# Optimization experiments

Hardware: AMD Instinct MI355X
Metric: run time of the kernel (lower is better)

The kernel has to match this reference:

```python
import jax, jax.numpy as jnp
import numpy as np

N = 30          # n_particles
H = 32          # h_dim
D = 3           # input_dim
B = 1024        # batch of point clouds


def _make_edge_index():
    # fully connected, no self loops; rows = [source j, target i] (PyG convention)
    pairs = np.array([[m, n] for m in range(N) for n in range(N) if m != n], dtype=np.int64)
    return jnp.asarray(pairs.T)  # [2, 870]


def setup_inputs() -> dict:
    key = jax.random.key(0)
    ks = jax.random.split(key, 13)
    p = lambda k, shp: jax.random.normal(k, shp, dtype=jnp.float32) * 0.05
    return {
        "x": jax.random.normal(ks[0], (B, N, D), dtype=jnp.float32),
        "W1": p(ks[1], (2 * D, H)), "b1": p(ks[2], (H,)),
        "W2": p(ks[3], (H, H)),     "b2": p(ks[4], (H,)),
        "W3": p(ks[5], (H, H)),     "b3": p(ks[6], (H,)),
        "W4": p(ks[7], (2 * H, H)), "b4": p(ks[8], (H,)),
        "W5": p(ks[9], (H, H)),     "b5": p(ks[10], (H,)),
        "W6": p(ks[11], (H, D)),    "b6": p(ks[12], (D,)),
        "edge_index": _make_edge_index(),
    }


def _mlp(m, Wa, ba, Wb, bb, Wc, bc):
    h = jax.nn.relu(m @ Wa + ba)
    h = jax.nn.relu(h @ Wb + bb)
    return h @ Wc + bc


def _edge_conv(x, src, dst, Wa, ba, Wb, bb, Wc, bc):
    # x: [B, N, F]. PyG EdgeConv: msg = nn(cat[x_i, x_j - x_i]), mean over incoming edges at i.
    xi = x[:, dst]                               # [B, E, F]
    xj = x[:, src]                               # [B, E, F]
    msg = _mlp(jnp.concatenate([xi, xj - xi], axis=-1), Wa, ba, Wb, bb, Wc, bc)  # [B, E, Fout]
    n_nodes = x.shape[1]
    agg = jnp.zeros((x.shape[0], n_nodes, msg.shape[-1]), msg.dtype).at[:, dst].add(msg)
    cnt = jnp.zeros((n_nodes,), msg.dtype).at[dst].add(1.0)
    return agg / jnp.maximum(cnt, 1.0)[:, None]


def reference(x, W1, b1, W2, b2, W3, b3, W4, b4, W5, b5, W6, b6, edge_index):
    src, dst = edge_index[0], edge_index[1]
    h = _edge_conv(x, src, dst, W1, b1, W2, b2, W3, b3)   # [B, N, H]
    out = _edge_conv(h, src, dst, W4, b4, W5, b5, W6, b6)  # [B, N, D]
    return out
```

## Files before the change

### kernel.cpp

```cpp
#include <hip/hip_runtime.h>
#include <hip/hip_bf16.h>

namespace {

typedef __attribute__((ext_vector_type(8))) short short8;
typedef __attribute__((ext_vector_type(16))) float float16v;

constexpr int N = 30;
constexpr int H = 32;
constexpr int D = 3;
constexpr int PW = H + 4;
constexpr float INV_CNT = 1.0f / 29.0f;

__device__ __forceinline__ short bfb(float x) {
    __hip_bfloat16 h = __float2bfloat16(x);
    return __builtin_bit_cast(short, h);
}

__device__ __forceinline__ float16v mfma32(short8 a, short8 b, float16v c) {
    return __builtin_amdgcn_mfma_f32_32x32x16_bf16(a, b, c, 0, 0, 0);
}

__global__ __launch_bounds__(256, 4) void gnn2_v2(
    const float* __restrict__ x,
    const float* __restrict__ W1, const float* __restrict__ b1,
    const float* __restrict__ W2, const float* __restrict__ b2,
    const float* __restrict__ W3, const float* __restrict__ b3,
    const float* __restrict__ W4, const float* __restrict__ b4,
    const float* __restrict__ W5, const float* __restrict__ b5,
    const float* __restrict__ W6, const float* __restrict__ b6,
    float* __restrict__ out)
{
    __shared__ float uS[32 * PW];
    __shared__ float vS[32 * PW];
    __shared__ float aggS[32 * PW];
    __shared__ float t2S[4][32 * PW];

    const int b    = blockIdx.x;
    const int t    = threadIdx.x;
    const int lane = t & 63;
    const int w    = t >> 6;
    const int col  = lane & 31;
    const int h    = lane >> 5;
    const int j    = col;

    short8 W2lo, W2hi, W3lo, W3hi, W5lo, W5hi, W6lo, W6hi;
#pragma unroll
    for (int e = 0; e < 8; ++e) {
        const int klo = 8 * h + e, khi = 16 + 8 * h + e;
        W2lo[e] = bfb(W2[klo * H + col]);  W2hi[e] = bfb(W2[khi * H + col]);
        W3lo[e] = bfb(W3[klo * H + col]);  W3hi[e] = bfb(W3[khi * H + col]);
        W5lo[e] = bfb(W5[klo * H + col]);  W5hi[e] = bfb(W5[khi * H + col]);
        W6lo[e] = bfb(col < D ? W6[klo * D + col] : 0.0f);
        W6hi[e] = bfb(col < D ? W6[khi * D + col] : 0.0f);
    }
    const float bb2 = b2[col], bb5 = b5[col], b3c = b3[col];
    const float b6c = (col < D) ? b6[col] : 0.0f;

    const float* xb = x + b * (N * D);
    if (t < N * 8) {
        const int i = t >> 3, gg = t & 7;
        const float x0 = xb[i*D+0], x1 = xb[i*D+1], x2 = xb[i*D+2];
#pragma unroll
        for (int ff = 0; ff < 4; ++ff) {
            const int f = gg + 8 * ff;
            const float wa0 = W1[0*H+f], wa1 = W1[1*H+f], wa2 = W1[2*H+f];
            const float wb0 = W1[3*H+f], wb1 = W1[4*H+f], wb2 = W1[5*H+f];
            vS[i*PW+f] = x0*wb0 + x1*wb1 + x2*wb2;
            uS[i*PW+f] = x0*(wa0-wb0) + x1*(wa1-wb1) + x2*(wa2-wb2) + b1[f];
        }
    }
    __syncthreads();

    float* const rt = t2S[w];

    {
        float vlo[8], vhi[8];
#pragma unroll
        for (int e = 0; e < 8; ++e) {
            vlo[e] = vS[j*PW + 8*h + e];
            vhi[e] = vS[j*PW + 16 + 8*h + e];
        }
#pragma unroll 1
        for (int i = w; i < N; i += 4) {
            const bool alive = (j < N) && (j != i);
            const float* ur = &uS[i*PW];
            short8 alo, ahi;
#pragma unroll
            for (int e = 0; e < 8; ++e) {
                const float t0 = fmaxf(ur[8*h + e]      + vlo[e], 0.0f);
                const float t1 = fmaxf(ur[16 + 8*h + e] + vhi[e], 0.0f);
                alo[e] = alive ? bfb(t0) : (short)0;
                ahi[e] = alive ? bfb(t1) : (short)0;
            }
            float16v acc;
#pragma unroll
            for (int r = 0; r < 16; ++r) acc[r] = bb2;
            acc = mfma32(alo, W2lo, acc);
            acc = mfma32(ahi, W2hi, acc);
#pragma unroll
            for (int r = 0; r < 16; ++r)
                rt[((r&3) + 8*(r>>2) + 4*h) * PW + col] = fmaxf(acc[r], 0.0f);
            short8 clo, chi;
#pragma unroll
            for (int e = 0; e < 8; ++e) {
                const float t0 = rt[j*PW + 8*h + e];
                const float t1 = rt[j*PW + 16 + 8*h + e];
                clo[e] = alive ? bfb(t0) : (short)0;
                chi[e] = alive ? bfb(t1) : (short)0;
            }
            float16v a2;
#pragma unroll
            for (int r = 0; r < 16; ++r) a2[r] = 0.0f;
            a2 = mfma32(clo, W3lo, a2);
            a2 = mfma32(chi, W3hi, a2);
            float s = 0.0f;
#pragma unroll
            for (int r = 0; r < 16; ++r) s += a2[r];
            s += __shfl_xor(s, 32, 64);
            if (h == 0) aggS[i*PW + col] = s * INV_CNT + b3c;
        }
    }
    __syncthreads();

    if (w < 2) {
        const bool aliveC = (j < N);
        short8 alo, ahi;
#pragma unroll
        for (int e = 0; e < 8; ++e) {
            const float t0 = aggS[j*PW + 8*h + e];
            const float t1 = aggS[j*PW + 16 + 8*h + e];
            alo[e] = aliveC ? bfb(t0) : (short)0;
            ahi[e] = aliveC ? bfb(t1) : (short)0;
        }
        short8 Flo, Fhi;
        float binit;
        if (w == 0) {
#pragma unroll
            for (int e = 0; e < 8; ++e) {
                const int klo = 8*h + e, khi = 16 + 8*h + e;
                Flo[e] = bfb(W4[klo*H + col] - W4[(H + klo)*H + col]);
                Fhi[e] = bfb(W4[khi*H + col] - W4[(H + khi)*H + col]);
            }
            binit = b4[col];
        } else {
#pragma unroll
            for (int e = 0; e < 8; ++e) {
                const int klo = 8*h + e, khi = 16 + 8*h + e;
                Flo[e] = bfb(W4[(H + klo)*H + col]);
                Fhi[e] = bfb(W4[(H + khi)*H + col]);
            }
            binit = 0.0f;
        }
        float16v acc;
#pragma unroll
        for (int r = 0; r < 16; ++r) acc[r] = binit;
        acc = mfma32(alo, Flo, acc);
        acc = mfma32(ahi, Fhi, acc);
        float* const dst = (w == 0) ? uS : vS;
#pragma unroll
        for (int r = 0; r < 16; ++r)
            dst[((r&3) + 8*(r>>2) + 4*h) * PW + col] = acc[r];
    }
    __syncthreads();

    {
        float vlo[8], vhi[8];
#pragma unroll
        for (int e = 0; e < 8; ++e) {
            vlo[e] = vS[j*PW + 8*h + e];
            vhi[e] = vS[j*PW + 16 + 8*h + e];
        }
#pragma unroll 1
        for (int i = w; i < N; i += 4) {
            const bool alive = (j < N) && (j != i);
            const float* ur = &uS[i*PW];
            short8 alo, ahi;
#pragma unroll
            for (int e = 0; e < 8; ++e) {
                const float t0 = fmaxf(ur[8*h + e]      + vlo[e], 0.0f);
                const float t1 = fmaxf(ur[16 + 8*h + e] + vhi[e], 0.0f);
                alo[e] = alive ? bfb(t0) : (short)0;
                ahi[e] = alive ? bfb(t1) : (short)0;
            }
            float16v acc;
#pragma unroll
            for (int r = 0; r < 16; ++r) acc[r] = bb5;
            acc = mfma32(alo, W5lo, acc);
            acc = mfma32(ahi, W5hi, acc);
#pragma unroll
            for (int r = 0; r < 16; ++r)
                rt[((r&3) + 8*(r>>2) + 4*h) * PW + col] = fmaxf(acc[r], 0.0f);
            short8 clo, chi;
#pragma unroll
            for (int e = 0; e < 8; ++e) {
                const float t0 = rt[j*PW + 8*h + e];
                const float t1 = rt[j*PW + 16 + 8*h + e];
                clo[e] = alive ? bfb(t0) : (short)0;
                chi[e] = alive ? bfb(t1) : (short)0;
            }
            float16v a2;
#pragma unroll
            for (int r = 0; r < 16; ++r) a2[r] = 0.0f;
            a2 = mfma32(clo, W6lo, a2);
            a2 = mfma32(chi, W6hi, a2);
            float s = 0.0f;
#pragma unroll
            for (int r = 0; r < 16; ++r) s += a2[r];
            s += __shfl_xor(s, 32, 64);
            if (lane < D) out[b*(N*D) + i*D + lane] = s * INV_CNT + b6c;
        }
    }
}

}

extern "C" void kernel_launch(void* const* d_in, const int* in_sizes, int n_in,
                              void* d_out, int out_size, void* d_ws, size_t ws_size,
                              hipStream_t stream) {
    const float* x  = (const float*)d_in[0];
    const float* W1 = (const float*)d_in[1];
    const float* b1 = (const float*)d_in[2];
    const float* W2 = (const float*)d_in[3];
    const float* b2 = (const float*)d_in[4];
    const float* W3 = (const float*)d_in[5];
    const float* b3 = (const float*)d_in[6];
    const float* W4 = (const float*)d_in[7];
    const float* b4 = (const float*)d_in[8];
    const float* W5 = (const float*)d_in[9];
    const float* b5 = (const float*)d_in[10];
    const float* W6 = (const float*)d_in[11];
    const float* b6 = (const float*)d_in[12];

    const int batch = in_sizes[0] / (N * D);
    float* out = (float*)d_out;

    gnn2_v2<<<dim3(batch), dim3(256), 0, stream>>>(
        x, W1, b1, W2, b2, W3, b3, W4, b4, W5, b5, W6, b6, out);
}
```

Measured before the change: 111.4 us.

## Swap MFMA operand order and pass intermediate activations through lane shuffles, not LDS

```diff
diff --git a/kernel.cpp b/kernel.cpp
--- a/kernel.cpp
+++ b/kernel.cpp
@@ -3,8 +3,10 @@
 
 namespace {
 
-typedef __attribute__((ext_vector_type(8))) short short8;
+typedef __attribute__((ext_vector_type(8)))  short short8;
 typedef __attribute__((ext_vector_type(16))) float float16v;
+typedef __attribute__((ext_vector_type(4)))  float f4;
+typedef __attribute__((ext_vector_type(4)))  int   int4v;
 
 constexpr int N = 30;
 constexpr int H = 32;
@@ -16,12 +18,16 @@
     __hip_bfloat16 h = __float2bfloat16(x);
     return __builtin_bit_cast(short, h);
 }
-
+__device__ __forceinline__ int pkbf(float a, float b) {
+    const unsigned lo = (unsigned short)bfb(a);
+    const unsigned hi = (unsigned short)bfb(b);
+    return (int)(lo | (hi << 16));
+}
 __device__ __forceinline__ float16v mfma32(short8 a, short8 b, float16v c) {
     return __builtin_amdgcn_mfma_f32_32x32x16_bf16(a, b, c, 0, 0, 0);
 }
 
-__global__ __launch_bounds__(256, 4) void gnn2_v2(
+__global__ __launch_bounds__(256, 4) void gnn2_v3(
     const float* __restrict__ x,
     const float* __restrict__ W1, const float* __restrict__ b1,
     const float* __restrict__ W2, const float* __restrict__ b2,
@@ -34,7 +40,6 @@
     __shared__ float uS[32 * PW];
     __shared__ float vS[32 * PW];
     __shared__ float aggS[32 * PW];
-    __shared__ float t2S[4][32 * PW];
 
     const int b    = blockIdx.x;
     const int t    = threadIdx.x;
@@ -44,18 +49,17 @@
     const int h    = lane >> 5;
     const int j    = col;
 
-    short8 W2lo, W2hi, W3lo, W3hi, W5lo, W5hi, W6lo, W6hi;
+    short8 W2lo, W2hi, W3lo, W3hi;
 #pragma unroll
     for (int e = 0; e < 8; ++e) {
         const int klo = 8 * h + e, khi = 16 + 8 * h + e;
         W2lo[e] = bfb(W2[klo * H + col]);  W2hi[e] = bfb(W2[khi * H + col]);
         W3lo[e] = bfb(W3[klo * H + col]);  W3hi[e] = bfb(W3[khi * H + col]);
-        W5lo[e] = bfb(W5[klo * H + col]);  W5hi[e] = bfb(W5[khi * H + col]);
-        W6lo[e] = bfb(col < D ? W6[klo * D + col] : 0.0f);
-        W6hi[e] = bfb(col < D ? W6[khi * D + col] : 0.0f);
-    }
-    const float bb2 = b2[col], bb5 = b5[col], b3c = b3[col];
-    const float b6c = (col < D) ? b6[col] : 0.0f;
+    }
+    float b2v[16];
+#pragma unroll
+    for (int r = 0; r < 16; ++r) b2v[r] = b2[(r & 3) + 8 * (r >> 2) + 4 * h];
+    const float b3c = b3[col];
 
     const float* xb = x + b * (N * D);
     if (t < N * 8) {
@@ -70,53 +74,70 @@
             uS[i*PW+f] = x0*(wa0-wb0) + x1*(wa1-wb1) + x2*(wa2-wb2) + b1[f];
         }
     }
+    if (t < 2 * PW) {
+        uS[30*PW + t] = 0.0f;  vS[30*PW + t] = 0.0f;  aggS[30*PW + t] = 0.0f;
+    }
     __syncthreads();
 
-    float* const rt = t2S[w];
-
     {
-        float vlo[8], vhi[8];
-#pragma unroll
-        for (int e = 0; e < 8; ++e) {
-            vlo[e] = vS[j*PW + 8*h + e];
-            vhi[e] = vS[j*PW + 16 + 8*h + e];
-        }
+        const f4 v0 = *(const f4*)&vS[j*PW + 8*h];
+        const f4 v1 = *(const f4*)&vS[j*PW + 8*h + 4];
+        const f4 v2 = *(const f4*)&vS[j*PW + 16 + 8*h];
+        const f4 v3 = *(const f4*)&vS[j*PW + 16 + 8*h + 4];
 #pragma unroll 1
         for (int i = w; i < N; i += 4) {
             const bool alive = (j < N) && (j != i);
             const float* ur = &uS[i*PW];
-            short8 alo, ahi;
-#pragma unroll
-            for (int e = 0; e < 8; ++e) {
-                const float t0 = fmaxf(ur[8*h + e]      + vlo[e], 0.0f);
-                const float t1 = fmaxf(ur[16 + 8*h + e] + vhi[e], 0.0f);
-                alo[e] = alive ? bfb(t0) : (short)0;
-                ahi[e] = alive ? bfb(t1) : (short)0;
-            }
+            const f4 u0 = *(const f4*)(ur + 8*h);
+            const f4 u1 = *(const f4*)(ur + 8*h + 4);
+            const f4 u2 = *(const f4*)(ur + 16 + 8*h);
+            const f4 u3 = *(const f4*)(ur + 16 + 8*h + 4);
+            const short8 alo = __builtin_bit_cast(short8, (int4v){
+                pkbf(fmaxf(u0[0]+v0[0],0.f), fmaxf(u0[1]+v0[1],0.f)),
+                pkbf(fmaxf(u0[2]+v0[2],0.f), fmaxf(u0[3]+v0[3],0.f)),
+                pkbf(fmaxf(u1[0]+v1[0],0.f), fmaxf(u1[1]+v1[1],0.f)),
+                pkbf(fmaxf(u1[2]+v1[2],0.f), fmaxf(u1[3]+v1[3],0.f))});
+            const short8 ahi = __builtin_bit_cast(short8, (int4v){
+                pkbf(fmaxf(u2[0]+v2[0],0.f), fmaxf(u2[1]+v2[1],0.f)),
+                pkbf(fmaxf(u2[2]+v2[2],0.f), fmaxf(u2[3]+v2[3],0.f)),
+                pkbf(fmaxf(u3[0]+v3[0],0.f), fmaxf(u3[1]+v3[1],0.f)),
+                pkbf(fmaxf(u3[2]+v3[2],0.f), fmaxf(u3[3]+v3[3],0.f))});
             float16v acc;
 #pragma unroll
-            for (int r = 0; r < 16; ++r) acc[r] = bb2;
-            acc = mfma32(alo, W2lo, acc);
-            acc = mfma32(ahi, W2hi, acc);
-#pragma unroll
-            for (int r = 0; r < 16; ++r)
-                rt[((r&3) + 8*(r>>2) + 4*h) * PW + col] = fmaxf(acc[r], 0.0f);
-            short8 clo, chi;
-#pragma unroll
-            for (int e = 0; e < 8; ++e) {
-                const float t0 = rt[j*PW + 8*h + e];
-                const float t1 = rt[j*PW + 16 + 8*h + e];
-                clo[e] = alive ? bfb(t0) : (short)0;
-                chi[e] = alive ? bfb(t1) : (short)0;
-            }
-            float16v a2;
-#pragma unroll
-            for (int r = 0; r < 16; ++r) a2[r] = 0.0f;
-            a2 = mfma32(clo, W3lo, a2);
-            a2 = mfma32(chi, W3hi, a2);
+            for (int r = 0; r < 16; ++r) acc[r] = b2v[r];
+            acc = mfma32(W2lo, alo, acc);
+            acc = mfma32(W2hi, ahi, acc);
+            const int P0 = pkbf(fmaxf(acc[0], 0.f), fmaxf(acc[1], 0.f));
+            const int P1 = pkbf(fmaxf(acc[2], 0.f), fmaxf(acc[3], 0.f));
+            const int P2 = pkbf(fmaxf(acc[4], 0.f), fmaxf(acc[5], 0.f));
+            const int P3 = pkbf(fmaxf(acc[6], 0.f), fmaxf(acc[7], 0.f));
+            const int P4 = pkbf(fmaxf(acc[8], 0.f), fmaxf(acc[9], 0.f));
+            const int P5 = pkbf(fmaxf(acc[10],0.f), fmaxf(acc[11],0.f));
+            const int P6 = pkbf(fmaxf(acc[12],0.f), fmaxf(acc[13],0.f));
+            const int P7 = pkbf(fmaxf(acc[14],0.f), fmaxf(acc[15],0.f));
+            const int sp0 = __shfl_xor(P0, 32, 64);
+            const int sp1 = __shfl_xor(P1, 32, 64);
+            const int sp2 = __shfl_xor(P2, 32, 64);
+            const int sp3 = __shfl_xor(P3, 32, 64);
+            const int sp4 = __shfl_xor(P4, 32, 64);
+            const int sp5 = __shfl_xor(P5, 32, 64);
+            const int sp6 = __shfl_xor(P6, 32, 64);
+            const int sp7 = __shfl_xor(P7, 32, 64);
+            int w0 = h ? sp2 : P0;  int w1 = h ? sp3 : P1;
+            int w2 = h ? P2 : sp0;  int w3 = h ? P3 : sp1;
+            int w4 = h ? sp6 : P4;  int w5 = h ? sp7 : P5;
+            int w6 = h ? P6 : sp4;  int w7 = h ? P7 : sp5;
+            if (!alive) { w0=0; w1=0; w2=0; w3=0; w4=0; w5=0; w6=0; w7=0; }
+            const short8 a2lo = __builtin_bit_cast(short8, (int4v){w0, w1, w2, w3});
+            const short8 a2hi = __builtin_bit_cast(short8, (int4v){w4, w5, w6, w7});
+            float16v m2;
+#pragma unroll
+            for (int r = 0; r < 16; ++r) m2[r] = 0.0f;
+            m2 = mfma32(a2lo, W3lo, m2);
+            m2 = mfma32(a2hi, W3hi, m2);
             float s = 0.0f;
 #pragma unroll
-            for (int r = 0; r < 16; ++r) s += a2[r];
+            for (int r = 0; r < 16; ++r) s += m2[r];
             s += __shfl_xor(s, 32, 64);
             if (h == 0) aggS[i*PW + col] = s * INV_CNT + b3c;
         }
@@ -164,49 +185,78 @@
     }
     __syncthreads();
 
+    short8 W5lo, W5hi, W6lo, W6hi;
+#pragma unroll
+    for (int e = 0; e < 8; ++e) {
+        const int klo = 8 * h + e, khi = 16 + 8 * h + e;
+        W5lo[e] = bfb(W5[klo * H + col]);  W5hi[e] = bfb(W5[khi * H + col]);
+        W6lo[e] = bfb(col < D ? W6[klo * D + col] : 0.0f);
+        W6hi[e] = bfb(col < D ? W6[khi * D + col] : 0.0f);
+    }
+    float b5v[16];
+#pragma unroll
+    for (int r = 0; r < 16; ++r) b5v[r] = b5[(r & 3) + 8 * (r >> 2) + 4 * h];
+    const float b6c = (col < D) ? b6[col] : 0.0f;
+
     {
-        float vlo[8], vhi[8];
-#pragma unroll
-        for (int e = 0; e < 8; ++e) {
-            vlo[e] = vS[j*PW + 8*h + e];
-            vhi[e] = vS[j*PW + 16 + 8*h + e];
-        }
+        const f4 v0 = *(const f4*)&vS[j*PW + 8*h];
+        const f4 v1 = *(const f4*)&vS[j*PW + 8*h + 4];
+        const f4 v2 = *(const f4*)&vS[j*PW + 16 + 8*h];
+        const f4 v3 = *(const f4*)&vS[j*PW + 16 + 8*h + 4];
 #pragma unroll 1
         for (int i = w; i < N; i += 4) {
             const bool alive = (j < N) && (j != i);
             const float* ur = &uS[i*PW];
-            short8 alo, ahi;
-#pragma unroll
-            for (int e = 0; e < 8; ++e) {
-                const float t0 = fmaxf(ur[8*h + e]      + vlo[e], 0.0f);
-                const float t1 = fmaxf(ur[16 + 8*h + e] + vhi[e], 0.0f);
-                alo[e] = alive ? bfb(t0) : (short)0;
-                ahi[e] = alive ? bfb(t1) : (short)0;
-            }
+            const f4 u0 = *(const f4*)(ur + 8*h);
+            const f4 u1 = *(const f4*)(ur + 8*h + 4);
+            const f4 u2 = *(const f4*)(ur + 16 + 8*h);
+            const f4 u3 = *(const f4*)(ur + 16 + 8*h + 4);
+            const short8 alo = __builtin_bit_cast(short8, (int4v){
+                pkbf(fmaxf(u0[0]+v0[0],0.f), fmaxf(u0[1]+v0[1],0.f)),
+                pkbf(fmaxf(u0[2]+v0[2],0.f), fmaxf(u0[3]+v0[3],0.f)),
+                pkbf(fmaxf(u1[0]+v1[0],0.f), fmaxf(u1[1]+v1[1],0.f)),
+                pkbf(fmaxf(u1[2]+v1[2],0.f), fmaxf(u1[3]+v1[3],0.f))});
+            const short8 ahi = __builtin_bit_cast(short8, (int4v){
+                pkbf(fmaxf(u2[0]+v2[0],0.f), fmaxf(u2[1]+v2[1],0.f)),
+                pkbf(fmaxf(u2[2]+v2[2],0.f), fmaxf(u2[3]+v2[3],0.f)),
+                pkbf(fmaxf(u3[0]+v3[0],0.f), fmaxf(u3[1]+v3[1],0.f)),
+                pkbf(fmaxf(u3[2]+v3[2],0.f), fmaxf(u3[3]+v3[3],0.f))});
             float16v acc;
 #pragma unroll
-            for (int r = 0; r < 16; ++r) acc[r] = bb5;
-            acc = mfma32(alo, W5lo, acc);
-            acc = mfma32(ahi, W5hi, acc);
-#pragma unroll
-            for (int r = 0; r < 16; ++r)
-                rt[((r&3) + 8*(r>>2) + 4*h) * PW + col] = fmaxf(acc[r], 0.0f);
-            short8 clo, chi;
-#pragma unroll
-            for (int e = 0; e < 8; ++e) {
-                const float t0 = rt[j*PW + 8*h + e];
-                const float t1 = rt[j*PW + 16 + 8*h + e];
-                clo[e] = alive ? bfb(t0) : (short)0;
-                chi[e] = alive ? bfb(t1) : (short)0;
-            }
-            float16v a2;
-#pragma unroll
-            for (int r = 0; r < 16; ++r) a2[r] = 0.0f;
-            a2 = mfma32(clo, W6lo, a2);
-            a2 = mfma32(chi, W6hi, a2);
+            for (int r = 0; r < 16; ++r) acc[r] = b5v[r];
+            acc = mfma32(W5lo, alo, acc);
+            acc = mfma32(W5hi, ahi, acc);
+            const int P0 = pkbf(fmaxf(acc[0], 0.f), fmaxf(acc[1], 0.f));
+            const int P1 = pkbf(fmaxf(acc[2], 0.f), fmaxf(acc[3], 0.f));
+            const int P2 = pkbf(fmaxf(acc[4], 0.f), fmaxf(acc[5], 0.f));
+            const int P3 = pkbf(fmaxf(acc[6], 0.f), fmaxf(acc[7], 0.f));
+            const int P4 = pkbf(fmaxf(acc[8], 0.f), fmaxf(acc[9], 0.f));
+            const int P5 = pkbf(fmaxf(acc[10],0.f), fmaxf(acc[11],0.f));
+            const int P6 = pkbf(fmaxf(acc[12],0.f), fmaxf(acc[13],0.f));
+            const int P7 = pkbf(fmaxf(acc[14],0.f), fmaxf(acc[15],0.f));
+            const int sp0 = __shfl_xor(P0, 32, 64);
+            const int sp1 = __shfl_xor(P1, 32, 64);
+            const int sp2 = __shfl_xor(P2, 32, 64);
+            const int sp3 = __shfl_xor(P3, 32, 64);
+            const int sp4 = __shfl_xor(P4, 32, 64);
+            const int sp5 = __shfl_xor(P5, 32, 64);
+            const int sp6 = __shfl_xor(P6, 32, 64);
+            const int sp7 = __shfl_xor(P7, 32, 64);
+            int w0 = h ? sp2 : P0;  int w1 = h ? sp3 : P1;
+            int w2 = h ? P2 : sp0;  int w3 = h ? P3 : sp1;
+            int w4 = h ? sp6 : P4;  int w5 = h ? sp7 : P5;
+            int w6 = h ? P6 : sp4;  int w7 = h ? P7 : sp5;
+            if (!alive) { w0=0; w1=0; w2=0; w3=0; w4=0; w5=0; w6=0; w7=0; }
+            const short8 a2lo = __builtin_bit_cast(short8, (int4v){w0, w1, w2, w3});
+            const short8 a2hi = __builtin_bit_cast(short8, (int4v){w4, w5, w6, w7});
+            float16v m2;
+#pragma unroll
+            for (int r = 0; r < 16; ++r) m2[r] = 0.0f;
+            m2 = mfma32(a2lo, W6lo, m2);
+            m2 = mfma32(a2hi, W6hi, m2);
             float s = 0.0f;
 #pragma unroll
-            for (int r = 0; r < 16; ++r) s += a2[r];
+            for (int r = 0; r < 16; ++r) s += m2[r];
             s += __shfl_xor(s, 32, 64);
             if (lane < D) out[b*(N*D) + i*D + lane] = s * INV_CNT + b6c;
         }
@@ -235,6 +285,6 @@
     const int batch = in_sizes[0] / (N * D);
     float* out = (float*)d_out;
 
-    gnn2_v2<<<dim3(batch), dim3(256), 0, stream>>>(
+    gnn2_v3<<<dim3(batch), dim3(256), 0, stream>>>(
         x, W1, b1, W2, b2, W3, b3, W4, b4, W5, b5, W6, b6, out);
 }
```

After: 103.2 us. 1.08x faster.
